# Kernel tuning notes

Hardware: AMD Instinct MI355X
Metric: run time of the kernel (lower is better)

The kernel has to match this reference:

```python
import jax, jax.numpy as jnp
import numpy as np


def setup_inputs() -> dict:
    key = jax.random.key(0)
    ks = jax.random.split(key, 5)
    B, Lq, Lkv, E, H = 4, 4096, 4096, 1024, 128
    x = jax.random.normal(ks[0], (B, Lq, E), dtype=jnp.float32)
    z = jax.random.normal(ks[1], (B, Lkv, E), dtype=jnp.float32)
    s = 1.0 / np.sqrt(E)
    Wq = jax.random.normal(ks[2], (H, E), dtype=jnp.float32) * s
    Wk = jax.random.normal(ks[3], (H, E), dtype=jnp.float32) * s
    Wv = jax.random.normal(ks[4], (H, E), dtype=jnp.float32) * s
    return {"x": x, "z": z, "Wq": Wq, "Wk": Wk, "Wv": Wv}


def reference(x, z, Wq, Wk, Wv):
    # q: [B, Lq, H]; k, v: [B, Lkv, H]  (torch Linear: y = x @ W.T)
    q = jnp.einsum('bqe,he->bqh', x, Wq)
    k = jnp.einsum('bke,he->bkh', z, Wk)
    v = jnp.einsum('bke,he->bkh', z, Wv)
    # NOTE: original code MULTIPLIES by sqrt(head_dim) (faithful reproduction)
    scale = jnp.asarray(k.shape[-1], x.dtype) ** 0.5
    weights = jnp.einsum('bqh,bkh->bqk', q, k) * scale  # [B, Lq, Lkv]
    weights = jax.nn.softmax(weights, axis=-1)
    logits = jnp.einsum('bqk,bkh->bqh', weights, v)  # [B, Lq, H]
    return logits
```

## Files before the change

kernel.cpp:

```cpp
#include <hip/hip_runtime.h>

typedef __attribute__((ext_vector_type(8))) short short8;
typedef __attribute__((ext_vector_type(4))) float f32x4;
typedef __attribute__((ext_vector_type(4))) float float4v;
typedef __attribute__((ext_vector_type(4))) unsigned short ushort4v;
typedef unsigned int __attribute__((may_alias)) u32ma;

#define B_   4
#define LQ   4096
#define LKV  4096
#define E_   1024
#define H_   128
#define NSPLIT 4
#define KVSPL (LKV / NSPLIT)
#define NT    (KVSPL / 64)
#define WELEM (H_ * E_)

static __device__ __forceinline__ unsigned short bf16_rne(float f) {
    unsigned int u = __float_as_uint(f);
    u += 0x7fffu + ((u >> 16) & 1u);
    return (unsigned short)(u >> 16);
}
static __device__ __forceinline__ float bf16_tof(unsigned short h) {
    return __uint_as_float(((unsigned int)h) << 16);
}
static __device__ __forceinline__ f32x4 mfma16(short8 a, short8 b, f32x4 c) {
    return __builtin_amdgcn_mfma_f32_16x16x32_bf16(a, b, c, 0, 0, 0);
}
static __device__ __forceinline__ void gload16(const unsigned short* g, unsigned short* l) {
    __builtin_amdgcn_global_load_lds(
        (const __attribute__((address_space(1))) unsigned int*)g,
        (__attribute__((address_space(3))) unsigned int*)l, 16, 0, 0);
}

__global__ __launch_bounds__(256) void convert_w_kernel(
    const float* __restrict__ Wq, const float* __restrict__ Wk, const float* __restrict__ Wv,
    unsigned short* __restrict__ wqh, unsigned short* __restrict__ wql,
    unsigned short* __restrict__ wkh, unsigned short* __restrict__ wkl,
    unsigned short* __restrict__ wvh)
{
    const int kb = blockIdx.x;
    const int which = blockIdx.y;
    const float* W = (which == 0) ? Wq : (which == 1) ? Wk : Wv;
    unsigned short* outh = (which == 0) ? wqh : (which == 1) ? wkh : wvh;
    unsigned short* outl = (which == 0) ? wql : wkl;
    const int t = threadIdx.x;
#pragma unroll
    for (int i = 0; i < 4; ++i) {
        const int c = t * 4 + i;
        const int h = c >> 3;
        const int k = kb * 64 + (((c & 7) ^ (h & 7)) * 8);
        const float* src = W + (size_t)h * E_ + k;
        float4v v0 = *(const float4v*)(src);
        float4v v1 = *(const float4v*)(src + 4);
        short8 hi, lo;
#pragma unroll
        for (int e = 0; e < 4; ++e) {
            unsigned short h0 = bf16_rne(v0[e]);
            unsigned short h1 = bf16_rne(v1[e]);
            hi[e] = (short)h0; hi[e + 4] = (short)h1;
            lo[e] = (short)bf16_rne(v0[e] - bf16_tof(h0));
            lo[e + 4] = (short)bf16_rne(v1[e] - bf16_tof(h1));
        }
        *(short8*)&outh[(size_t)kb * 8192 + (size_t)c * 8] = hi;
        if (which < 2) *(short8*)&outl[(size_t)kb * 8192 + (size_t)c * 8] = lo;
    }
}

__global__ __launch_bounds__(512, 1) void proj_kernel(
    const float* __restrict__ x, const float* __restrict__ z,
    const unsigned short* __restrict__ wqh, const unsigned short* __restrict__ wql,
    const unsigned short* __restrict__ wkh, const unsigned short* __restrict__ wkl,
    const unsigned short* __restrict__ wvh,
    unsigned short* __restrict__ qhi, unsigned short* __restrict__ qlo,
    unsigned short* __restrict__ khi, unsigned short* __restrict__ klo,
    unsigned short* __restrict__ vt)
{
    const int bid = blockIdx.x;
    const bool qmode = bid < 128;
    const int m0 = (qmode ? bid : bid - 128) * 128;
    const float* Asrc = qmode ? x : z;
    const unsigned short* W1h = qmode ? wqh : wkh;
    const unsigned short* W1l = qmode ? wql : wkl;

    const int t = threadIdx.x;
    const int w = t >> 6, l = t & 63, lg = (l >> 4) & 3, ll = l & 15;
    const int mw = w & 3, nw = w >> 2;

    __shared__ unsigned short Ah[2][8192];
    __shared__ unsigned short Al[2][8192];
    __shared__ unsigned short Wh[2][8192];
    __shared__ unsigned short Wl[2][8192];
    __shared__ unsigned short Wv2[8192];

    const int ar = t >> 2, aq = t & 3;
    float4v ra[4];
    auto loadA = [&](int e0) {
        const float* p = Asrc + (size_t)(m0 + ar) * E_ + e0 + aq * 16;
#pragma unroll
        for (int i = 0; i < 4; ++i) ra[i] = *(const float4v*)(p + i * 4);
    };
    auto writeA = [&](int ab) {
#pragma unroll
        for (int half = 0; half < 2; ++half) {
            short8 hi, lo;
#pragma unroll
            for (int e = 0; e < 4; ++e) {
                float v0 = ra[2 * half][e];
                float v1 = ra[2 * half + 1][e];
                unsigned short h0 = bf16_rne(v0);
                unsigned short h1 = bf16_rne(v1);
                hi[e] = (short)h0; hi[e + 4] = (short)h1;
                lo[e] = (short)bf16_rne(v0 - bf16_tof(h0));
                lo[e + 4] = (short)bf16_rne(v1 - bf16_tof(h1));
            }
            const int j = 2 * aq + half;
            const int off = ar * 64 + ((j ^ (ar & 7)) * 8);
            *(short8*)&Ah[ab][off] = hi;
            *(short8*)&Al[ab][off] = lo;
        }
    };
    auto issueW = [&](int kb, int bsel) {
#pragma unroll
        for (int i = 0; i < 2; ++i) {
            const int cbase = w * 128 + i * 64;
            const size_t so = (size_t)kb * 8192 + (size_t)(cbase + l) * 8;
            gload16(W1h + so, &Wh[bsel][(size_t)cbase * 8]);
            gload16(W1l + so, &Wl[bsel][(size_t)cbase * 8]);
        }
    };
    auto issueWv = [&](int kb) {
#pragma unroll
        for (int i = 0; i < 2; ++i) {
            const int cbase = w * 128 + i * 64;
            const size_t so = (size_t)kb * 8192 + (size_t)(cbase + l) * 8;
            gload16(wvh + so, &Wv2[(size_t)cbase * 8]);
        }
    };

    f32x4 acc[2][4], accv[2][4];
    const f32x4 zz = {0.f, 0.f, 0.f, 0.f};
#pragma unroll
    for (int rf = 0; rf < 2; ++rf)
#pragma unroll
        for (int cf = 0; cf < 4; ++cf) { acc[rf][cf] = zz; accv[rf][cf] = zz; }

    loadA(0);
    issueW(0, 0);
    if (!qmode) issueWv(0);
    asm volatile("s_waitcnt vmcnt(0)" ::: "memory");
    writeA(0);
    asm volatile("s_waitcnt lgkmcnt(0)" ::: "memory");
    __builtin_amdgcn_s_barrier();

    for (int kb = 0; kb < 16; ++kb) {
        const int cur = kb & 1;
        if (kb < 15) {
            loadA((kb + 1) * 64);
            issueW(kb + 1, cur ^ 1);
        }

#pragma unroll
        for (int ks = 0; ks < 2; ++ks) {
            short8 a_h[2], a_l[2];
#pragma unroll
            for (int rf = 0; rf < 2; ++rf) {
                const int r = mw * 32 + rf * 16 + ll;
                const int off = r * 64 + (((ks * 4 + lg) ^ (ll & 7)) * 8);
                a_h[rf] = *(const short8*)&Ah[cur][off];
                a_l[rf] = *(const short8*)&Al[cur][off];
            }
#pragma unroll
            for (int cf = 0; cf < 4; ++cf) {
                const int hrow = nw * 64 + cf * 16 + ll;
                const int off = hrow * 64 + (((ks * 4 + lg) ^ (ll & 7)) * 8);
                short8 bh = *(const short8*)&Wh[cur][off];
                short8 bl = *(const short8*)&Wl[cur][off];
#pragma unroll
                for (int rf = 0; rf < 2; ++rf) {
                    acc[rf][cf] = mfma16(a_h[rf], bh, acc[rf][cf]);
                    acc[rf][cf] = mfma16(a_h[rf], bl, acc[rf][cf]);
                    acc[rf][cf] = mfma16(a_l[rf], bh, acc[rf][cf]);
                }
                if (!qmode) {
                    short8 bv = *(const short8*)&Wv2[off];
#pragma unroll
                    for (int rf = 0; rf < 2; ++rf)
                        accv[rf][cf] = mfma16(a_h[rf], bv, accv[rf][cf]);
                }
            }
        }

        if (kb < 15) {
            writeA(cur ^ 1);
            if (!qmode) issueWv(kb + 1);
            asm volatile("s_waitcnt vmcnt(0) lgkmcnt(0)" ::: "memory");
            __builtin_amdgcn_sched_barrier(0);
            __builtin_amdgcn_s_barrier();
        }
    }

#pragma unroll
    for (int rf = 0; rf < 2; ++rf)
#pragma unroll
        for (int cf = 0; cf < 4; ++cf)
#pragma unroll
            for (int j = 0; j < 4; ++j) {
                const int m = m0 + mw * 32 + rf * 16 + 4 * lg + j;
                const int h = nw * 64 + cf * 16 + ll;
                const float val = acc[rf][cf][j];
                unsigned short hi = bf16_rne(val);
                unsigned short lo = bf16_rne(val - bf16_tof(hi));
                const size_t o = (size_t)m * H_ + h;
                if (qmode) {
                    qhi[o] = hi; qlo[o] = lo;
                } else {
                    khi[o] = hi; klo[o] = lo;
                    const int b = m >> 12, kv = m & 4095;
                    vt[(size_t)b * ((size_t)H_ * LKV) + (size_t)h * LKV + kv] =
                        bf16_rne(accv[rf][cf][j]);
                }
            }
}

__global__ __launch_bounds__(256, 2) void attn_kernel(
    const unsigned short* __restrict__ qhi, const unsigned short* __restrict__ qlo,
    const unsigned short* __restrict__ khi, const unsigned short* __restrict__ klo,
    const unsigned short* __restrict__ vt,
    float* __restrict__ Opart, float* __restrict__ msb, float* __restrict__ lsb)
{
    const int blk = blockIdx.x;
    const int bb = blk & 3;
    const int qt = (blk >> 2) & 31;
    const int split = blk >> 7;
    const int t = threadIdx.x;
    const int w = t >> 6, l = t & 63, lg = (l >> 4) & 3, ll = l & 15;

    __shared__ unsigned short Kh[8192];
    __shared__ unsigned short Kl[8192];
    __shared__ unsigned short Vb[8192];
    __shared__ unsigned short Pl[4][32][64];

    const float CSC = 11.313708498984761f * 1.4426950408889634f;

    short8 qh[2][4], ql[2][4];
#pragma unroll
    for (int b = 0; b < 2; ++b) {
        const size_t qrow = (size_t)(bb * LQ + qt * 128 + w * 32 + b * 16 + ll) * H_;
#pragma unroll
        for (int ks = 0; ks < 4; ++ks) {
            qh[b][ks] = *(const short8*)(qhi + qrow + ks * 32 + lg * 8);
            ql[b][ks] = *(const short8*)(qlo + qrow + ks * 32 + lg * 8);
        }
    }

    const int kv_base = split * KVSPL;
    const unsigned short* khb = khi + (size_t)bb * LKV * H_;
    const unsigned short* klb = klo + (size_t)bb * LKV * H_;
    const unsigned short* vbg = vt + (size_t)bb * ((size_t)H_ * LKV);

    auto issue_K = [&](int kv0) {
#pragma unroll
        for (int ci = 0; ci < 4; ++ci) {
            const int chunk = w * 4 + ci;
            const int row = chunk * 4 + (l >> 4);
            const int c = l & 15;
            const size_t so = (size_t)(kv0 + row) * H_ + ((c ^ (row & 7)) * 8);
            gload16(khb + so, &Kh[chunk * 512]);
            gload16(klb + so, &Kl[chunk * 512]);
        }
    };
    auto issue_V = [&](int kv0) {
#pragma unroll
        for (int ci = 0; ci < 4; ++ci) {
            const int chunk = w * 4 + ci;
            const int row = chunk * 8 + (l >> 3);
            const int c = l & 7;
            gload16(vbg + (size_t)row * LKV + kv0 + ((c ^ (row & 7)) * 8),
                    &Vb[chunk * 512]);
        }
    };

    f32x4 O[8][2];
    const f32x4 zz = {0.f, 0.f, 0.f, 0.f};
#pragma unroll
    for (int f = 0; f < 8; ++f) { O[f][0] = zz; O[f][1] = zz; }
    float mold[2] = {-1e30f, -1e30f};
    float lsum[2] = {0.f, 0.f};

    issue_K(kv_base);
    issue_V(kv_base);
    asm volatile("s_waitcnt vmcnt(0)" ::: "memory");
    __builtin_amdgcn_s_barrier();

    for (int ti = 0; ti < NT; ++ti) {
        f32x4 S[4][2];
#pragma unroll
        for (int a = 0; a < 4; ++a) { S[a][0] = zz; S[a][1] = zz; }
        __builtin_amdgcn_s_setprio(1);
#pragma unroll
        for (int ks = 0; ks < 4; ++ks) {
#pragma unroll
            for (int a = 0; a < 4; ++a) {
                const int row = a * 16 + ll;
                const int off = row * 128 + (((ks * 4 + lg) ^ (ll & 7)) * 8);
                short8 kh  = *(const short8*)&Kh[off];
                short8 kl2 = *(const short8*)&Kl[off];
                S[a][0] = mfma16(kh,  qh[0][ks], S[a][0]);
                S[a][0] = mfma16(kh,  ql[0][ks], S[a][0]);
                S[a][0] = mfma16(kl2, qh[0][ks], S[a][0]);
                S[a][1] = mfma16(kh,  qh[1][ks], S[a][1]);
                S[a][1] = mfma16(kh,  ql[1][ks], S[a][1]);
                S[a][1] = mfma16(kl2, qh[1][ks], S[a][1]);
            }
        }
        __builtin_amdgcn_s_setprio(0);

        float crr[2];
#pragma unroll
        for (int b = 0; b < 2; ++b) {
            float mx = S[0][b][0];
#pragma unroll
            for (int a = 0; a < 4; ++a)
#pragma unroll
                for (int j = 0; j < 4; ++j) mx = fmaxf(mx, S[a][b][j]);
            mx = fmaxf(mx, __shfl_xor(mx, 16));
            mx = fmaxf(mx, __shfl_xor(mx, 32));
            float mn = fmaxf(mold[b], mx * CSC);
            float corr = exp2f(mold[b] - mn);
            float ps = 0.f;
#pragma unroll
            for (int a = 0; a < 4; ++a) {
                float p0 = exp2f(fmaf(S[a][b][0], CSC, -mn));
                float p1 = exp2f(fmaf(S[a][b][1], CSC, -mn));
                float p2 = exp2f(fmaf(S[a][b][2], CSC, -mn));
                float p3 = exp2f(fmaf(S[a][b][3], CSC, -mn));
                ps += (p0 + p1) + (p2 + p3);
                unsigned int pk0, pk1;
                asm("v_cvt_pk_bf16_f32 %0, %1, %2" : "=v"(pk0) : "v"(p0), "v"(p1));
                asm("v_cvt_pk_bf16_f32 %0, %1, %2" : "=v"(pk1) : "v"(p2), "v"(p3));
                const int row = b * 16 + ll;
                u32ma* pd = (u32ma*)&Pl[w][0][0];
                const int di = row * 32 + (((2 * a + (lg >> 1)) ^ (ll & 7)) * 4) + 2 * (lg & 1);
                pd[di] = pk0;
                pd[di + 1] = pk1;
            }
            ps += __shfl_xor(ps, 16);
            ps += __shfl_xor(ps, 32);
            lsum[b] = lsum[b] * corr + ps;
            mold[b] = mn;
            crr[b] = corr;
        }
#pragma unroll
        for (int f = 0; f < 8; ++f) {
            O[f][0] *= crr[0];
            O[f][1] *= crr[1];
        }

        asm volatile("s_waitcnt vmcnt(0) lgkmcnt(0)" ::: "memory");
        __builtin_amdgcn_sched_barrier(0);
        __builtin_amdgcn_s_barrier();
        if (ti + 1 < NT) issue_K(kv_base + (ti + 1) * 64);
        __builtin_amdgcn_sched_barrier(0);

        __builtin_amdgcn_s_setprio(1);
#pragma unroll
        for (int ks = 0; ks < 2; ++ks) {
            short8 pb[2];
#pragma unroll
            for (int b = 0; b < 2; ++b) {
                const int row = b * 16 + ll;
                pb[b] = *(const short8*)&Pl[w][row][((ks * 4 + lg) ^ (ll & 7)) * 8];
            }
#pragma unroll
            for (int f = 0; f < 8; ++f) {
                const int row = f * 16 + ll;
                short8 va = *(const short8*)&Vb[row * 64
                                               + (((ks * 4 + lg) ^ (ll & 7)) * 8)];
                O[f][0] = mfma16(va, pb[0], O[f][0]);
                O[f][1] = mfma16(va, pb[1], O[f][1]);
            }
        }
        __builtin_amdgcn_s_setprio(0);

        __builtin_amdgcn_s_barrier();
        if (ti + 1 < NT) issue_V(kv_base + (ti + 1) * 64);
        asm volatile("s_waitcnt vmcnt(4)" ::: "memory");
        __builtin_amdgcn_sched_barrier(0);
        __builtin_amdgcn_s_barrier();
    }

    const size_t obase = ((((size_t)split * 4 + bb) * 32 + qt) * 4 + w) * 16;
#pragma unroll
    for (int f = 0; f < 8; ++f)
#pragma unroll
        for (int b = 0; b < 2; ++b)
            *(float4v*)&Opart[(obase + f * 2 + b) * 256 + l * 4] = O[f][b];

    if (lg == 0) {
#pragma unroll
        for (int b = 0; b < 2; ++b) {
            const int q = qt * 128 + w * 32 + b * 16 + ll;
            msb[((size_t)split * 4 + bb) * LQ + q] = mold[b];
            lsb[((size_t)split * 4 + bb) * LQ + q] = lsum[b];
        }
    }
}

__global__ __launch_bounds__(512) void combine_kernel(
    const float* __restrict__ Opart, const float* __restrict__ msb,
    const float* __restrict__ lsb, float* __restrict__ out)
{
    const int blk = blockIdx.x;
    const int bb = blk & 3;
    const int qt = (blk >> 2) & 31;
    const int fg = blk >> 7;
    const int t = threadIdx.x;
    const int w = t >> 6, l = t & 63, lg = (l >> 4) & 3, ll = l & 15;
    const int wq = w & 3, wf = w >> 2;

#pragma unroll
    for (int b = 0; b < 2; ++b) {
        const int q = qt * 128 + wq * 32 + b * 16 + ll;
        float ms[NSPLIT], ls[NSPLIT];
#pragma unroll
        for (int s = 0; s < NSPLIT; ++s) {
            ms[s] = msb[((size_t)s * 4 + bb) * LQ + q];
            ls[s] = lsb[((size_t)s * 4 + bb) * LQ + q];
        }
        float mM = fmaxf(fmaxf(ms[0], ms[1]), fmaxf(ms[2], ms[3]));
        float wsp[NSPLIT];
        float L = 0.f;
#pragma unroll
        for (int s = 0; s < NSPLIT; ++s) {
            wsp[s] = exp2f(ms[s] - mM);
            L += ls[s] * wsp[s];
        }
        const float inv = 1.f / L;
#pragma unroll
        for (int fi = 0; fi < 2; ++fi) {
            const int f = fg * 4 + wf * 2 + fi;
            f32x4 acc = {0.f, 0.f, 0.f, 0.f};
#pragma unroll
            for (int s = 0; s < NSPLIT; ++s) {
                const size_t ob = ((((size_t)s * 4 + bb) * 32 + qt) * 4 + wq) * 16 + f * 2 + b;
                float4v ov = *(const float4v*)&Opart[ob * 256 + l * 4];
#pragma unroll
                for (int j = 0; j < 4; ++j) acc[j] += ov[j] * wsp[s];
            }
#pragma unroll
            for (int j = 0; j < 4; ++j) acc[j] *= inv;
            *(float4v*)&out[((size_t)bb * LQ + q) * H_ + f * 16 + lg * 4] = acc;
        }
    }
}

extern "C" void kernel_launch(void* const* d_in, const int* in_sizes, int n_in,
                              void* d_out, int out_size, void* d_ws, size_t ws_size,
                              hipStream_t stream) {
    const float* x  = (const float*)d_in[0];
    const float* z  = (const float*)d_in[1];
    const float* Wq = (const float*)d_in[2];
    const float* Wk = (const float*)d_in[3];
    const float* Wv = (const float*)d_in[4];
    float* out = (float*)d_out;

    const size_t NQ = (size_t)B_ * LQ * H_;
    unsigned short* qhi = (unsigned short*)d_ws;
    unsigned short* qlo = qhi + NQ;
    unsigned short* khi = qlo + NQ;
    unsigned short* klo = khi + NQ;
    unsigned short* vtp = klo + NQ;
    float* Opart = (float*)(vtp + NQ);
    float* msb   = Opart + (size_t)NSPLIT * NQ;
    float* lsb   = msb + (size_t)NSPLIT * B_ * LQ;
    unsigned short* wqh = (unsigned short*)(lsb + (size_t)NSPLIT * B_ * LQ);
    unsigned short* wql = wqh + WELEM;
    unsigned short* wkh = wql + WELEM;
    unsigned short* wkl = wkh + WELEM;
    unsigned short* wvh = wkl + WELEM;

    convert_w_kernel<<<dim3(16, 3), 256, 0, stream>>>(Wq, Wk, Wv, wqh, wql, wkh, wkl, wvh);
    proj_kernel<<<dim3(256), 512, 0, stream>>>(x, z, wqh, wql, wkh, wkl, wvh,
                                               qhi, qlo, khi, klo, vtp);
    attn_kernel<<<dim3(512), 256, 0, stream>>>(qhi, qlo, khi, klo, vtp, Opart, msb, lsb);
    combine_kernel<<<dim3(256), 512, 0, stream>>>(Opart, msb, lsb, out);
}
```

Baseline: 135.4 us.

## Fuse split-KV combine into attention kernel via last-block atomic counter

Removes the separate combine kernel launch. Each attention block increments a per-(batch, q-tile) counter after writing its partial output, and the last of the four splits performs the softmax merge and writes the final output. The counters are zeroed in the weight-conversion kernel. This trades one launch and its tail gap for threadfences, an atomic, and a serialized combine tail inside the attention blocks.

```diff
diff --git a/kernel.cpp b/kernel.cpp
--- a/kernel.cpp
+++ b/kernel.cpp
@@ -37,7 +37,7 @@
     const float* __restrict__ Wq, const float* __restrict__ Wk, const float* __restrict__ Wv,
     unsigned short* __restrict__ wqh, unsigned short* __restrict__ wql,
     unsigned short* __restrict__ wkh, unsigned short* __restrict__ wkl,
-    unsigned short* __restrict__ wvh)
+    unsigned short* __restrict__ wvh, unsigned int* __restrict__ cnt)
 {
     const int kb = blockIdx.x;
     const int which = blockIdx.y;
@@ -45,6 +45,7 @@
     unsigned short* outh = (which == 0) ? wqh : (which == 1) ? wkh : wvh;
     unsigned short* outl = (which == 0) ? wql : wkl;
     const int t = threadIdx.x;
+    if (kb == 0 && which == 0 && t < 128) cnt[t] = 0u;
 #pragma unroll
     for (int i = 0; i < 4; ++i) {
         const int c = t * 4 + i;
@@ -227,7 +228,8 @@
     const unsigned short* __restrict__ qhi, const unsigned short* __restrict__ qlo,
     const unsigned short* __restrict__ khi, const unsigned short* __restrict__ klo,
     const unsigned short* __restrict__ vt,
-    float* __restrict__ Opart, float* __restrict__ msb, float* __restrict__ lsb)
+    float* __restrict__ Opart, float* __restrict__ msb, float* __restrict__ lsb,
+    float* __restrict__ out, unsigned int* __restrict__ cnt)
 {
     const int blk = blockIdx.x;
     const int bb = blk & 3;
@@ -240,6 +242,7 @@
     __shared__ unsigned short Kl[8192];
     __shared__ unsigned short Vb[8192];
     __shared__ unsigned short Pl[4][32][64];
+    __shared__ unsigned int sflag;
 
     const float CSC = 11.313708498984761f * 1.4426950408889634f;
 
@@ -405,52 +408,49 @@
             lsb[((size_t)split * 4 + bb) * LQ + q] = lsum[b];
         }
     }
-}
-
-__global__ __launch_bounds__(512) void combine_kernel(
-    const float* __restrict__ Opart, const float* __restrict__ msb,
-    const float* __restrict__ lsb, float* __restrict__ out)
-{
-    const int blk = blockIdx.x;
-    const int bb = blk & 3;
-    const int qt = (blk >> 2) & 31;
-    const int fg = blk >> 7;
-    const int t = threadIdx.x;
-    const int w = t >> 6, l = t & 63, lg = (l >> 4) & 3, ll = l & 15;
-    const int wq = w & 3, wf = w >> 2;
-
-#pragma unroll
-    for (int b = 0; b < 2; ++b) {
-        const int q = qt * 128 + wq * 32 + b * 16 + ll;
-        float ms[NSPLIT], ls[NSPLIT];
-#pragma unroll
-        for (int s = 0; s < NSPLIT; ++s) {
-            ms[s] = msb[((size_t)s * 4 + bb) * LQ + q];
-            ls[s] = lsb[((size_t)s * 4 + bb) * LQ + q];
-        }
-        float mM = fmaxf(fmaxf(ms[0], ms[1]), fmaxf(ms[2], ms[3]));
-        float wsp[NSPLIT];
-        float L = 0.f;
-#pragma unroll
-        for (int s = 0; s < NSPLIT; ++s) {
-            wsp[s] = exp2f(ms[s] - mM);
-            L += ls[s] * wsp[s];
-        }
-        const float inv = 1.f / L;
-#pragma unroll
-        for (int fi = 0; fi < 2; ++fi) {
-            const int f = fg * 4 + wf * 2 + fi;
-            f32x4 acc = {0.f, 0.f, 0.f, 0.f};
+
+    __syncthreads();
+    __threadfence();
+    if (t == 0) {
+        unsigned int old = atomicAdd(&cnt[(bb << 5) + qt], 1u);
+        sflag = (old == 3u) ? 1u : 0u;
+    }
+    __syncthreads();
+    if (sflag) {
+        __threadfence();
+#pragma unroll
+        for (int b = 0; b < 2; ++b) {
+            const int q = qt * 128 + w * 32 + b * 16 + ll;
+            float ms[NSPLIT], ls[NSPLIT];
 #pragma unroll
             for (int s = 0; s < NSPLIT; ++s) {
-                const size_t ob = ((((size_t)s * 4 + bb) * 32 + qt) * 4 + wq) * 16 + f * 2 + b;
-                float4v ov = *(const float4v*)&Opart[ob * 256 + l * 4];
-#pragma unroll
-                for (int j = 0; j < 4; ++j) acc[j] += ov[j] * wsp[s];
-            }
-#pragma unroll
-            for (int j = 0; j < 4; ++j) acc[j] *= inv;
-            *(float4v*)&out[((size_t)bb * LQ + q) * H_ + f * 16 + lg * 4] = acc;
+                ms[s] = msb[((size_t)s * 4 + bb) * LQ + q];
+                ls[s] = lsb[((size_t)s * 4 + bb) * LQ + q];
+            }
+            float mM = fmaxf(fmaxf(ms[0], ms[1]), fmaxf(ms[2], ms[3]));
+            float wsp[NSPLIT];
+            float L = 0.f;
+#pragma unroll
+            for (int s = 0; s < NSPLIT; ++s) {
+                wsp[s] = exp2f(ms[s] - mM);
+                L += ls[s] * wsp[s];
+            }
+            const float inv = 1.f / L;
+#pragma unroll
+            for (int f = 0; f < 8; ++f) {
+                f32x4 acc = {0.f, 0.f, 0.f, 0.f};
+#pragma unroll
+                for (int s = 0; s < NSPLIT; ++s) {
+                    const size_t ob = ((((size_t)s * 4 + bb) * 32 + qt) * 4 + w) * 16
+                                    + f * 2 + b;
+                    float4v ov = *(const float4v*)&Opart[ob * 256 + l * 4];
+#pragma unroll
+                    for (int j = 0; j < 4; ++j) acc[j] += ov[j] * wsp[s];
+                }
+#pragma unroll
+                for (int j = 0; j < 4; ++j) acc[j] *= inv;
+                *(float4v*)&out[((size_t)bb * LQ + q) * H_ + f * 16 + lg * 4] = acc;
+            }
         }
     }
 }
@@ -479,10 +479,12 @@
     unsigned short* wkh = wql + WELEM;
     unsigned short* wkl = wkh + WELEM;
     unsigned short* wvh = wkl + WELEM;
-
-    convert_w_kernel<<<dim3(16, 3), 256, 0, stream>>>(Wq, Wk, Wv, wqh, wql, wkh, wkl, wvh);
+    unsigned int* cnt = (unsigned int*)(wvh + WELEM);
+
+    convert_w_kernel<<<dim3(16, 3), 256, 0, stream>>>(Wq, Wk, Wv, wqh, wql, wkh,
+                                                      wkl, wvh, cnt);
     proj_kernel<<<dim3(256), 512, 0, stream>>>(x, z, wqh, wql, wkh, wkl, wvh,
                                                qhi, qlo, khi, klo, vtp);
-    attn_kernel<<<dim3(512), 256, 0, stream>>>(qhi, qlo, khi, klo, vtp, Opart, msb, lsb);
-    combine_kernel<<<dim3(256), 512, 0, stream>>>(Opart, msb, lsb, out);
-}
+    attn_kernel<<<dim3(512), 256, 0, stream>>>(qhi, qlo, khi, klo, vtp,
+                                               Opart, msb, lsb, out, cnt);
+}
```

Result: slower. 198.5 us (+46.7%).
